# Kernel optimization log

Measured on AMD Instinct MI355X. Metric: run time of the kernel, lower is better.

The kernel has to match this reference:

```python
import jax, jax.numpy as jnp
import numpy as np

EOS = 0
INCLUDE_EOS = True
INS_COST = 1.0
DEL_COST = 1.0
SUB_COST = 1.0


def _seq_lens(tok):
    # tok: (T, N) int tokens; length = index of first EOS (+1 if included), else T
    T = tok.shape[0]
    is_eos = tok == EOS
    has = is_eos.any(axis=0)
    idx = jnp.argmax(is_eos, axis=0)
    return jnp.where(has, idx + (1 if INCLUDE_EOS else 0), T)


def _edit_distance(ref, hyp, ref_lens, hyp_lens):
    # ref: (R, N), hyp: (H, N). Levenshtein DP, scan over hyp steps.
    # The sequential deletion dependence along the ref axis is turned into a
    # min-plus prefix scan: new_row[j] = j*del + cummin_k<=j (cand[k] - k*del).
    R, N = ref.shape
    H = hyp.shape[0]
    offs = (jnp.arange(R + 1, dtype=jnp.float32) * DEL_COST)[:, None]  # (R+1,1)
    row0 = jnp.broadcast_to(offs, (R + 1, N)) + jnp.zeros((R + 1, N), jnp.float32)

    def step(row, xs):
        i, h = xs  # i: 1-based hyp step, h: (N,) hyp tokens at this step
        sub_c = SUB_COST * (ref != h[None, :]).astype(jnp.float32)  # (R,N)
        cand = jnp.concatenate(
            [row[:1] + INS_COST,
             jnp.minimum(row[1:] + INS_COST, row[:-1] + sub_c)], axis=0)
        new_row = jax.lax.cummin(cand - offs, axis=0) + offs
        # freeze rows for sequences whose hypothesis already ended
        row = jnp.where(i <= hyp_lens[None, :], new_row, row)
        return row, None

    row, _ = jax.lax.scan(step, row0, (jnp.arange(1, H + 1), hyp))
    # distance at (hyp_len, ref_len) per sequence
    return jnp.take_along_axis(row, ref_lens[None, :], axis=0)[0]


def setup_inputs() -> dict:
    key = jax.random.key(0)
    k1, k2, k3 = jax.random.split(key, 3)
    log_probs = jax.random.normal(k1, (128, 64), dtype=jnp.float32)
    ref = jax.random.randint(k2, (256, 128), 0, 1000, dtype=jnp.int64)
    hyp = jax.random.randint(k3, (256, 128, 64), 0, 1000, dtype=jnp.int64)
    return {"log_probs": log_probs, "ref": ref, "hyp": hyp}


def reference(log_probs, ref, hyp):
    batch_size, samples = log_probs.shape
    R = ref.shape[0]
    H = hyp.shape[0]
    # ref is 2D: broadcast across samples (same reference per batch element)
    ref_flat = jnp.repeat(ref[:, :, None], samples, axis=2).reshape(R, batch_size * samples)
    hyp_flat = hyp.reshape(H, batch_size * samples)
    ref_lens = _seq_lens(ref_flat)
    hyp_lens = _seq_lens(hyp_flat)
    dist = _edit_distance(ref_flat, hyp_flat, ref_lens, hyp_lens)
    er = dist / ref_lens.astype(jnp.float32)  # norm=True -> error rate
    er = er.reshape(batch_size, samples)
    er = er - er.mean(axis=1, keepdims=True)  # sub_avg=True
    loss = er * jax.nn.softmax(log_probs, axis=1)
    return loss.mean()  # reduction='mean'
```

## Files before the change

### kernel.cpp

```cpp
#include <hip/hip_runtime.h>
#include <stdint.h>


#define BATCH   128
#define SAMPLES 64
#define RLEN    256
#define HLEN    256
#define NSEQ    (BATCH*SAMPLES)
#define NTOK    1000
#define NWW     8
#define SPB     32
#define PMSTR   9
#define HTROW   260
#define RSTEP   4
#define NPH     72

typedef unsigned long long u64;
typedef unsigned int       u32;

__device__ __forceinline__ int row_shr1(int x) {
    return __builtin_amdgcn_mov_dpp(x, 0x111, 0xf, 0xf, true);
}

__global__ __launch_bounds__(256) void mer_edit(const int* __restrict__ ref,
                                                const int* __restrict__ hyp,
                                                int* __restrict__ scores,
                                                int* __restrict__ reflen)
{
    const int blk  = blockIdx.x;
    const int b    = blk >> 1;
    const int half = blk & 1;
    const int tid  = threadIdx.x;
    const int w    = tid & 7;
    const int sl   = tid >> 3;

    __shared__ __align__(16) u32 pm[NTOK * PMSTR];
    __shared__ __align__(8)  unsigned short ht[SPB * HTROW];
    __shared__ int m_sh;

    if (tid == 0) m_sh = RLEN;

    for (int i = tid; i < (NTOK * PMSTR) / 4; i += 256)
        ((int4*)pm)[i] = int4{0, 0, 0, 0};

#pragma unroll
    for (int it = 0; it < 8; it++) {
        int idx = it * 256 + tid;
        int t   = idx >> 3;
        int s4  = (idx & 7) * 4;
        int4 v  = *(const int4*)(hyp + t * NSEQ + b * SAMPLES + half * SPB + s4);
        ht[(s4 + 0) * HTROW + t] = (unsigned short)v.x;
        ht[(s4 + 1) * HTROW + t] = (unsigned short)v.y;
        ht[(s4 + 2) * HTROW + t] = (unsigned short)v.z;
        ht[(s4 + 3) * HTROW + t] = (unsigned short)v.w;
    }

    const int rt = ref[tid * BATCH + b];
    __syncthreads();
    if (rt == 0) atomicMin(&m_sh, tid);
    __syncthreads();
    const int m = (m_sh < RLEN) ? (m_sh + 1) : RLEN;
    if (tid < m)
        atomicOr(&pm[rt * PMSTR + (tid >> 5)], 1u << (tid & 31));
    __syncthreads();

    const int  sw   = (m - 1) >> 5, sb = (m - 1) & 31;
    const bool isW0 = (w == 0);
    const bool isSW = (w == sw);
    const u32* pmw   = pm + w;
    const unsigned short* htrow = ht + sl * HTROW;

    u32  VP = ~0u, VN = 0u;
    int  score = m;
    bool done  = false;

    int base = -(w << 2);

    int c0 = base     < 0 ? 0 : base;
    int c1 = base + 4 < 0 ? 0 : base + 4;
    uint2 tkA = *(const uint2*)(htrow + c0);
    uint2 tkB = *(const uint2*)(htrow + c1);
    u32 eqA0, eqA1, eqA2, eqA3;
    {
        u32 p0 = tkA.x & 0xFFFFu, p1 = tkA.x >> 16;
        u32 p2 = tkA.y & 0xFFFFu, p3 = tkA.y >> 16;
        eqA0 = pmw[p0 * PMSTR]; eqA1 = pmw[p1 * PMSTR];
        eqA2 = pmw[p2 * PMSTR]; eqA3 = pmw[p3 * PMSTR];
    }

    int out_pkd = 0;

#define STEP(EQ, TK, I) do {                                              \
        u32 cin  = ((u32)inp >> (I)) & 1u;                                \
        u32 hpin = ((u32)inp >> (8 + (I))) & 1u;                          \
        u32 hnin = ((u32)inp >> (16 + (I))) & 1u;                         \
        u32 x  = (EQ) & VP;                                               \
        u64 S  = (u64)x + VP + cin;                                       \
        u32 s2 = (u32)S;                                                  \
        u32 D0 = (s2 ^ VP) | (EQ) | VN;                                   \
        u32 HP = VN | ~(D0 | VP);                                         \
        u32 HN = VP & D0;                                                 \
        nout |= ((u32)(S >> 32) << (I)) | ((HP >> 31) << (8 + (I)))       \
                | ((HN >> 31) << (16 + (I)));                             \
        int delta = (int)((HP >> sb) & 1u) - (int)((HN >> sb) & 1u);      \
        u32 HPs = (HP << 1) | hpin;                                       \
        u32 HNs = (HN << 1) | hnin;                                       \
        if (pvalid) {                                                     \
            VP = HNs | ~(D0 | HPs);                                       \
            VN = HPs & D0;                                                \
            if (!done) {                                                  \
                score += delta;                                           \
                if ((TK) == 0) done = true;    \
            }                                                             \
        }                                                                 \
    } while (0)

#pragma unroll 2
    for (int P = 0; P < NPH; ++P) {
        int tl = base + 8;
        tl = tl < 0 ? 0 : (tl > (HLEN - RSTEP) ? (HLEN - RSTEP) : tl);
        uint2 tkC = *(const uint2*)(htrow + tl);

        u32 n0 = tkB.x & 0xFFFFu, n1 = tkB.x >> 16;
        u32 n2 = tkB.y & 0xFFFFu, n3 = tkB.y >> 16;
        u32 eqB0 = pmw[n0 * PMSTR], eqB1 = pmw[n1 * PMSTR];
        u32 eqB2 = pmw[n2 * PMSTR], eqB3 = pmw[n3 * PMSTR];

        int inp = row_shr1(out_pkd);
        if (isW0) inp = 0x0F00;

        const bool pvalid = ((u32)base < (u32)HLEN);
        u32 nout = 0;
        u32 a0 = tkA.x & 0xFFFFu, a1 = tkA.x >> 16;
        u32 a2 = tkA.y & 0xFFFFu, a3 = tkA.y >> 16;
        STEP(eqA0, a0, 0);
        STEP(eqA1, a1, 1);
        STEP(eqA2, a2, 2);
        STEP(eqA3, a3, 3);
        out_pkd = (int)nout;

        tkA = tkB; tkB = tkC;
        eqA0 = eqB0; eqA1 = eqB1; eqA2 = eqB2; eqA3 = eqB3;
        base += RSTEP;
    }
#undef STEP

    if (isSW) scores[b * SAMPLES + half * SPB + sl] = score;
    if (half == 0 && tid == 0) reflen[b] = m;
}

__global__ __launch_bounds__(64) void mer_loss(const float* __restrict__ lp,
                                               const int* __restrict__ scores,
                                               const int* __restrict__ reflen,
                                               double* __restrict__ partial)
{
    const int b = blockIdx.x, s = threadIdx.x;
    double er = (double)scores[b * SAMPLES + s] / (double)reflen[b];
    double x  = (double)lp[b * SAMPLES + s];
    double mx = x;
#pragma unroll
    for (int off = 32; off > 0; off >>= 1)
        mx = fmax(mx, __shfl_xor(mx, off));
    double e = exp(x - mx);
    double se = e, see = er * e, ser = er;
#pragma unroll
    for (int off = 32; off > 0; off >>= 1) {
        se  += __shfl_xor(se,  off);
        see += __shfl_xor(see, off);
        ser += __shfl_xor(ser, off);
    }
    if (s == 0) partial[b] = see / se - ser * (1.0 / SAMPLES);
}

__global__ __launch_bounds__(64) void mer_final(const double* __restrict__ partial,
                                                float* __restrict__ out)
{
    const int tid = threadIdx.x;
    double v = partial[tid] + partial[tid + 64];
#pragma unroll
    for (int off = 32; off > 0; off >>= 1)
        v += __shfl_xor(v, off);
    if (tid == 0) out[0] = (float)(v / (double)(BATCH * SAMPLES));
}

extern "C" void kernel_launch(void* const* d_in, const int* in_sizes, int n_in,
                              void* d_out, int out_size, void* d_ws, size_t ws_size,
                              hipStream_t stream)
{
    const float* lp  = (const float*)d_in[0];
    const int*   ref = (const int*)d_in[1];
    const int*   hyp = (const int*)d_in[2];

    double* partial = (double*)d_ws;
    int*    scores  = (int*)(partial + BATCH);
    int*    reflen  = scores + NSEQ;
    float*  out     = (float*)d_out;

    mer_edit<<<2 * BATCH, 256, 0, stream>>>(ref, hyp, scores, reflen);
    mer_loss<<<BATCH, 64, 0, stream>>>(lp, scores, reflen, partial);
    mer_final<<<1, 64, 0, stream>>>(partial, out);
}
```

Measured before the change: 92.60 us.

## Widen edit-distance wavefront to 8 hyp steps per phase and fuse tail kernels

The bit-parallel Myers wavefront now processes 8 hypothesis tokens per phase instead of 4, cutting the phase count from 72 to 39 and halving the number of cross-lane DPP exchanges. Hypothesis rows are padded with a sentinel token (1000) at the head and tail, which lets the per-step validity branch and index clamping be dropped. The pm table grows by one zeroed entry so the sentinel looks up an empty match mask. The two tail kernels (loss and final reduction) are merged into one 1024-thread block, saving a launch at the cost of a serial single-block reduction.

```diff
diff --git a/kernel.cpp b/kernel.cpp
--- a/kernel.cpp
+++ b/kernel.cpp
@@ -8,12 +8,13 @@
 #define HLEN    256
 #define NSEQ    (BATCH*SAMPLES)
 #define NTOK    1000
-#define NWW     8
+#define PADTOK  1000
 #define SPB     32
 #define PMSTR   9
-#define HTROW   260
-#define RSTEP   4
-#define NPH     72
+#define HEADPAD 56
+#define HTROW   392
+#define RSTEP   8
+#define NPH     39
 
 typedef unsigned long long u64;
 typedef unsigned int       u32;
@@ -34,14 +35,27 @@
     const int w    = tid & 7;
     const int sl   = tid >> 3;
 
-    __shared__ __align__(16) u32 pm[NTOK * PMSTR];
-    __shared__ __align__(8)  unsigned short ht[SPB * HTROW];
+    __shared__ __align__(16) u32 pm[9012];
+    __shared__ __align__(16) unsigned short ht[SPB * HTROW];
     __shared__ int m_sh;
 
     if (tid == 0) m_sh = RLEN;
 
-    for (int i = tid; i < (NTOK * PMSTR) / 4; i += 256)
+    for (int i = tid; i < 2253; i += 256)
         ((int4*)pm)[i] = int4{0, 0, 0, 0};
+
+    {
+        const int r = tid >> 3, c = tid & 7;
+        u32* rowp = (u32*)ht + r * (HTROW / 2);
+#pragma unroll
+        for (int j0 = 0; j0 < 9; ++j0) {
+            int j = c * 9 + j0;
+            if (j < 68) {
+                int off = (j < 28) ? j : (156 + (j - 28));
+                rowp[off] = 0x03E803E8u;
+            }
+        }
+    }
 
 #pragma unroll
     for (int it = 0; it < 8; it++) {
@@ -49,10 +63,10 @@
         int t   = idx >> 3;
         int s4  = (idx & 7) * 4;
         int4 v  = *(const int4*)(hyp + t * NSEQ + b * SAMPLES + half * SPB + s4);
-        ht[(s4 + 0) * HTROW + t] = (unsigned short)v.x;
-        ht[(s4 + 1) * HTROW + t] = (unsigned short)v.y;
-        ht[(s4 + 2) * HTROW + t] = (unsigned short)v.z;
-        ht[(s4 + 3) * HTROW + t] = (unsigned short)v.w;
+        ht[(s4 + 0) * HTROW + HEADPAD + t] = (unsigned short)v.x;
+        ht[(s4 + 1) * HTROW + HEADPAD + t] = (unsigned short)v.y;
+        ht[(s4 + 2) * HTROW + HEADPAD + t] = (unsigned short)v.z;
+        ht[(s4 + 3) * HTROW + HEADPAD + t] = (unsigned short)v.w;
     }
 
     const int rt = ref[tid * BATCH + b];
@@ -67,25 +81,28 @@
     const int  sw   = (m - 1) >> 5, sb = (m - 1) & 31;
     const bool isW0 = (w == 0);
     const bool isSW = (w == sw);
-    const u32* pmw   = pm + w;
-    const unsigned short* htrow = ht + sl * HTROW;
+    const u32* pmw  = pm + w;
+    const unsigned short* htrow = ht + sl * HTROW + HEADPAD;
 
     u32  VP = ~0u, VN = 0u;
     int  score = m;
     bool done  = false;
-
-    int base = -(w << 2);
-
-    int c0 = base     < 0 ? 0 : base;
-    int c1 = base + 4 < 0 ? 0 : base + 4;
-    uint2 tkA = *(const uint2*)(htrow + c0);
-    uint2 tkB = *(const uint2*)(htrow + c1);
-    u32 eqA0, eqA1, eqA2, eqA3;
+    int  base  = -(w << 3);
+
+    uint4 tkB;
+    u32 a0,a1,a2,a3,a4,a5,a6,a7;
+    u32 eqA0,eqA1,eqA2,eqA3,eqA4,eqA5,eqA6,eqA7;
     {
-        u32 p0 = tkA.x & 0xFFFFu, p1 = tkA.x >> 16;
-        u32 p2 = tkA.y & 0xFFFFu, p3 = tkA.y >> 16;
-        eqA0 = pmw[p0 * PMSTR]; eqA1 = pmw[p1 * PMSTR];
-        eqA2 = pmw[p2 * PMSTR]; eqA3 = pmw[p3 * PMSTR];
+        uint4 tkA = *(const uint4*)(htrow + base);
+        tkB = *(const uint4*)(htrow + base + 8);
+        a0 = tkA.x & 0xFFFFu; a1 = tkA.x >> 16;
+        a2 = tkA.y & 0xFFFFu; a3 = tkA.y >> 16;
+        a4 = tkA.z & 0xFFFFu; a5 = tkA.z >> 16;
+        a6 = tkA.w & 0xFFFFu; a7 = tkA.w >> 16;
+        eqA0 = pmw[a0 * PMSTR]; eqA1 = pmw[a1 * PMSTR];
+        eqA2 = pmw[a2 * PMSTR]; eqA3 = pmw[a3 * PMSTR];
+        eqA4 = pmw[a4 * PMSTR]; eqA5 = pmw[a5 * PMSTR];
+        eqA6 = pmw[a6 * PMSTR]; eqA7 = pmw[a7 * PMSTR];
     }
 
     int out_pkd = 0;
@@ -105,42 +122,45 @@
         int delta = (int)((HP >> sb) & 1u) - (int)((HN >> sb) & 1u);      \
         u32 HPs = (HP << 1) | hpin;                                       \
         u32 HNs = (HN << 1) | hnin;                                       \
-        if (pvalid) {                                                     \
-            VP = HNs | ~(D0 | HPs);                                       \
-            VN = HPs & D0;                                                \
-            if (!done) {                                                  \
-                score += delta;                                           \
-                if ((TK) == 0) done = true;    \
-            }                                                             \
-        }                                                                 \
+        VP = HNs | ~(D0 | HPs);                                           \
+        VN = HPs & D0;                                                    \
+        if (pvalid && !done) score += delta;                              \
+        done = done | ((TK) == 0);          \
     } while (0)
 
-#pragma unroll 2
+#pragma unroll 3
     for (int P = 0; P < NPH; ++P) {
-        int tl = base + 8;
-        tl = tl < 0 ? 0 : (tl > (HLEN - RSTEP) ? (HLEN - RSTEP) : tl);
-        uint2 tkC = *(const uint2*)(htrow + tl);
+        uint4 tkC = *(const uint4*)(htrow + base + 16);
 
         u32 n0 = tkB.x & 0xFFFFu, n1 = tkB.x >> 16;
         u32 n2 = tkB.y & 0xFFFFu, n3 = tkB.y >> 16;
+        u32 n4 = tkB.z & 0xFFFFu, n5 = tkB.z >> 16;
+        u32 n6 = tkB.w & 0xFFFFu, n7 = tkB.w >> 16;
         u32 eqB0 = pmw[n0 * PMSTR], eqB1 = pmw[n1 * PMSTR];
         u32 eqB2 = pmw[n2 * PMSTR], eqB3 = pmw[n3 * PMSTR];
+        u32 eqB4 = pmw[n4 * PMSTR], eqB5 = pmw[n5 * PMSTR];
+        u32 eqB6 = pmw[n6 * PMSTR], eqB7 = pmw[n7 * PMSTR];
 
         int inp = row_shr1(out_pkd);
-        if (isW0) inp = 0x0F00;
+        if (isW0) inp = 0xFF00;
 
         const bool pvalid = ((u32)base < (u32)HLEN);
         u32 nout = 0;
-        u32 a0 = tkA.x & 0xFFFFu, a1 = tkA.x >> 16;
-        u32 a2 = tkA.y & 0xFFFFu, a3 = tkA.y >> 16;
         STEP(eqA0, a0, 0);
         STEP(eqA1, a1, 1);
         STEP(eqA2, a2, 2);
         STEP(eqA3, a3, 3);
+        STEP(eqA4, a4, 4);
+        STEP(eqA5, a5, 5);
+        STEP(eqA6, a6, 6);
+        STEP(eqA7, a7, 7);
         out_pkd = (int)nout;
 
-        tkA = tkB; tkB = tkC;
+        a0 = n0; a1 = n1; a2 = n2; a3 = n3;
+        a4 = n4; a5 = n5; a6 = n6; a7 = n7;
         eqA0 = eqB0; eqA1 = eqB1; eqA2 = eqB2; eqA3 = eqB3;
+        eqA4 = eqB4; eqA5 = eqB5; eqA6 = eqB6; eqA7 = eqB7;
+        tkB = tkC;
         base += RSTEP;
     }
 #undef STEP
@@ -149,38 +169,44 @@
     if (half == 0 && tid == 0) reflen[b] = m;
 }
 
-__global__ __launch_bounds__(64) void mer_loss(const float* __restrict__ lp,
-                                               const int* __restrict__ scores,
-                                               const int* __restrict__ reflen,
-                                               double* __restrict__ partial)
-{
-    const int b = blockIdx.x, s = threadIdx.x;
-    double er = (double)scores[b * SAMPLES + s] / (double)reflen[b];
-    double x  = (double)lp[b * SAMPLES + s];
-    double mx = x;
-#pragma unroll
-    for (int off = 32; off > 0; off >>= 1)
-        mx = fmax(mx, __shfl_xor(mx, off));
-    double e = exp(x - mx);
-    double se = e, see = er * e, ser = er;
-#pragma unroll
-    for (int off = 32; off > 0; off >>= 1) {
-        se  += __shfl_xor(se,  off);
-        see += __shfl_xor(see, off);
-        ser += __shfl_xor(ser, off);
-    }
-    if (s == 0) partial[b] = see / se - ser * (1.0 / SAMPLES);
-}
-
-__global__ __launch_bounds__(64) void mer_final(const double* __restrict__ partial,
-                                                float* __restrict__ out)
+__global__ __launch_bounds__(1024) void mer_tail(const float* __restrict__ lp,
+                                                 const int* __restrict__ scores,
+                                                 const int* __restrict__ reflen,
+                                                 float* __restrict__ out)
 {
     const int tid = threadIdx.x;
-    double v = partial[tid] + partial[tid + 64];
-#pragma unroll
-    for (int off = 32; off > 0; off >>= 1)
-        v += __shfl_xor(v, off);
-    if (tid == 0) out[0] = (float)(v / (double)(BATCH * SAMPLES));
+    const int s   = tid & 63;
+    const int wv  = tid >> 6;
+    __shared__ double red[16];
+
+    double acc = 0.0;
+#pragma unroll
+    for (int k = 0; k < 8; k++) {
+        const int b  = wv * 8 + k;
+        double er = (double)scores[b * SAMPLES + s] / (double)reflen[b];
+        double x  = (double)lp[b * SAMPLES + s];
+        double mx = x;
+#pragma unroll
+        for (int off = 32; off > 0; off >>= 1)
+            mx = fmax(mx, __shfl_xor(mx, off));
+        double e = exp(x - mx);
+        double se = e, see = er * e, ser = er;
+#pragma unroll
+        for (int off = 32; off > 0; off >>= 1) {
+            se  += __shfl_xor(se,  off);
+            see += __shfl_xor(see, off);
+            ser += __shfl_xor(ser, off);
+        }
+        if (s == 0) acc += see / se - ser * (1.0 / SAMPLES);
+    }
+    if (s == 0) red[wv] = acc;
+    __syncthreads();
+    if (tid == 0) {
+        double v = 0.0;
+#pragma unroll
+        for (int i = 0; i < 16; i++) v += red[i];
+        out[0] = (float)(v / (double)(BATCH * SAMPLES));
+    }
 }
 
 extern "C" void kernel_launch(void* const* d_in, const int* in_sizes, int n_in,
@@ -191,12 +217,10 @@
     const int*   ref = (const int*)d_in[1];
     const int*   hyp = (const int*)d_in[2];
 
-    double* partial = (double*)d_ws;
-    int*    scores  = (int*)(partial + BATCH);
-    int*    reflen  = scores + NSEQ;
-    float*  out     = (float*)d_out;
+    int*   scores = (int*)d_ws;
+    int*   reflen = scores + NSEQ;
+    float* out    = (float*)d_out;
 
     mer_edit<<<2 * BATCH, 256, 0, stream>>>(ref, hyp, scores, reflen);
-    mer_loss<<<BATCH, 64, 0, stream>>>(lp, scores, reflen, partial);
-    mer_final<<<1, 64, 0, stream>>>(partial, out);
-}
+    mer_tail<<<1, 1024, 0, stream>>>(lp, scores, reflen, out);
+}
```

Result: slower. 105.2 us (+13.6%).
